# Optimization experiments

Hardware: AMD Instinct MI355X
Metric: run time of the kernel (lower is better)

Reference implementation:

```python
import jax, jax.numpy as jnp
import numpy as np

N_HEAD = 16
N_EMBD = 2048
HEAD_DIM = N_EMBD // N_HEAD
ROPE_BASE = 10000.0


def _rope_cos_sin(seq_len, dim, dtype):
    inv_freq = 1.0 / (ROPE_BASE ** (jnp.arange(0, dim, 2, dtype=jnp.float32) / dim))
    pos = jnp.arange(seq_len, dtype=jnp.float32)
    freqs = jnp.outer(pos, inv_freq)                 # [T, dim/2]
    emb = jnp.concatenate([freqs, freqs], axis=-1)   # [T, dim]
    return jnp.cos(emb).astype(dtype), jnp.sin(emb).astype(dtype)


def _rotate_half(x):
    x1, x2 = jnp.split(x, 2, axis=-1)
    return jnp.concatenate([-x2, x1], axis=-1)


def _apply_rotary(x, cos, sin):
    # x: [B, H, T, D]; cos/sin: [T, D] broadcast over B,H
    return x * cos[None, None] + _rotate_half(x) * sin[None, None]


def setup_inputs() -> dict:
    key = jax.random.key(0)
    ks = jax.random.split(key, 5)
    B, T, C = 4, 2048, N_EMBD
    s_in = 1.0 / np.sqrt(C)
    return {
        "x": jax.random.normal(ks[0], (B, T, C), dtype=jnp.float32),
        "W_attn": jax.random.normal(ks[1], (C, 3 * C), dtype=jnp.float32) * s_in,
        "b_attn": jax.random.normal(ks[2], (3 * C,), dtype=jnp.float32) * 0.02,
        "W_proj": jax.random.normal(ks[3], (C, C), dtype=jnp.float32) * s_in,
        "b_proj": jax.random.normal(ks[4], (C,), dtype=jnp.float32) * 0.02,
    }


def reference(x, W_attn, b_attn, W_proj, b_proj):
    B, T, C = x.shape
    H, D = N_HEAD, HEAD_DIM
    qkv = x @ W_attn + b_attn                        # [B, T, 3C]
    q, k, v = jnp.split(qkv, 3, axis=2)
    q = q.reshape(B, T, H, D).transpose(0, 2, 1, 3)  # [B, H, T, D]
    k = k.reshape(B, T, H, D).transpose(0, 2, 1, 3)
    v = v.reshape(B, T, H, D).transpose(0, 2, 1, 3)

    cos, sin = _rope_cos_sin(T, D, x.dtype)
    q = _apply_rotary(q, cos, sin)
    k = _apply_rotary(k, cos, sin)

    scale = 1.0 / jnp.sqrt(jnp.asarray(D, dtype=x.dtype))
    scores = jnp.einsum('bhqd,bhkd->bhqk', q, k) * scale
    causal = jnp.tril(jnp.ones((T, T), dtype=bool))
    scores = jnp.where(causal[None, None], scores, jnp.finfo(x.dtype).min)
    attn = jax.nn.softmax(scores, axis=-1)
    y = jnp.einsum('bhqk,bhkd->bhqd', attn, v)       # [B, H, T, D]
    y = y.transpose(0, 2, 1, 3).reshape(B, T, C)
    out = y @ W_proj + b_proj                        # dropout p=0 (eval)
    return out, k, v
```

## Files before the change

### kernel.cpp

```cpp
#include <hip/hip_runtime.h>


typedef __attribute__((ext_vector_type(4))) float f32x4;
typedef __attribute__((ext_vector_type(8))) __bf16 bf16x8;
typedef __attribute__((ext_vector_type(4))) unsigned short us4;

__device__ __forceinline__ unsigned short f2bf(float f) {
  unsigned u = __float_as_uint(f);
  u += 0x7FFFu + ((u >> 16) & 1u);
  return (unsigned short)(u >> 16);
}

__device__ __forceinline__ void gl_lds16(const void* g, void* l) {
  __builtin_amdgcn_global_load_lds(
      (const __attribute__((address_space(1))) void*)g,
      (__attribute__((address_space(3))) void*)l, 16, 0, 0);
}

__device__ __forceinline__ f32x4 mfma_bf16(bf16x8 a, bf16x8 b, f32x4 c) {
  return __builtin_amdgcn_mfma_f32_16x16x32_bf16(a, b, c, 0, 0, 0);
}


__global__ __launch_bounds__(256) void rope_table_kernel(float* __restrict__ cos_t,
                                                         float* __restrict__ sin_t) {
  int idx = blockIdx.x * 256 + threadIdx.x;
  int t = idx >> 6, i = idx & 63;
  float freq = __expf(-(float)i * 0.14391156831212787f);
  float ang = (float)t * freq;
  float s, c;
  sincosf(ang, &s, &c);
  cos_t[idx] = c;
  sin_t[idx] = s;
}

__global__ __launch_bounds__(256) void conv_bf16_kernel(const float* __restrict__ in,
                                                        unsigned short* __restrict__ out,
                                                        int n4) {
  int idx = blockIdx.x * 256 + threadIdx.x;
  int stride = gridDim.x * 256;
  for (; idx < n4; idx += stride) {
    float4 v = ((const float4*)in)[idx];
    us4 o;
    o[0] = f2bf(v.x); o[1] = f2bf(v.y); o[2] = f2bf(v.z); o[3] = f2bf(v.w);
    ((us4*)out)[idx] = o;
  }
}

__global__ __launch_bounds__(256) void transpose_conv_kernel(const float* __restrict__ in,
                                                             unsigned short* __restrict__ out,
                                                             int R, int C, int permute) {
  __shared__ unsigned short tile[64][68];
  const int t = threadIdx.x;
  const int c0 = blockIdx.x * 64, r0 = blockIdx.y * 64;
  const int cq = t & 15, rr = t >> 4;
#pragma unroll
  for (int i = 0; i < 4; ++i) {
    int r = rr + i * 16;
    float4 v = *(const float4*)&in[(size_t)(r0 + r) * C + c0 + cq * 4];
    tile[r][cq * 4 + 0] = f2bf(v.x);
    tile[r][cq * 4 + 1] = f2bf(v.y);
    tile[r][cq * 4 + 2] = f2bf(v.z);
    tile[r][cq * 4 + 3] = f2bf(v.w);
  }
  __syncthreads();
#pragma unroll
  for (int ii = 0; ii < 4; ++ii) {
    int c = rr + ii * 16;
    int n = c0 + c;
    int np = n;
    if (permute && n < 4096) {
      int d = n & 127, blk = d >> 5;
      int dd = (blk == 1) ? d + 32 : (blk == 2) ? d - 32 : d;
      np = (n & ~127) | dd;
    }
    us4 o;
#pragma unroll
    for (int jj = 0; jj < 4; ++jj) o[jj] = tile[cq * 4 + jj][c];
    *(us4*)&out[(size_t)np * R + r0 + cq * 4] = o;
  }
}

__global__ __launch_bounds__(256) void vtrans_kernel(const float* __restrict__ in,
                                                     unsigned short* __restrict__ out) {
  __shared__ unsigned short tile[64][68];
  const int t = threadIdx.x;
  const int t0 = blockIdx.x * 64;
  const int d0 = blockIdx.y * 64;
  const size_t zi = (size_t)blockIdx.z * 2048 * 128;
  const size_t zo = (size_t)blockIdx.z * 128 * 2048;
  const int cq = t & 15, rr = t >> 4;
#pragma unroll
  for (int i = 0; i < 4; ++i) {
    int r = rr + i * 16;
    float4 v = *(const float4*)&in[zi + (size_t)(t0 + r) * 128 + d0 + cq * 4];
    tile[r][cq * 4 + 0] = f2bf(v.x);
    tile[r][cq * 4 + 1] = f2bf(v.y);
    tile[r][cq * 4 + 2] = f2bf(v.z);
    tile[r][cq * 4 + 3] = f2bf(v.w);
  }
  __syncthreads();
#pragma unroll
  for (int ii = 0; ii < 4; ++ii) {
    int c = rr + ii * 16;
    us4 o;
#pragma unroll
    for (int jj = 0; jj < 4; ++jj) o[jj] = tile[cq * 4 + jj][c];
    *(us4*)&out[zo + (size_t)(d0 + c) * 2048 + t0 + cq * 4] = o;
  }
}


#define BARR __builtin_amdgcn_s_barrier()
#define LGKM                                                                   \
  do {                                                                         \
    asm volatile("s_waitcnt lgkmcnt(0)" ::: "memory");                         \
    __builtin_amdgcn_sched_barrier(0);                                         \
  } while (0)
#define WAITV(N) asm volatile("s_waitcnt vmcnt(" #N ")" ::: "memory")

#define STAGE_A_HALF(BUF, T, H)                                                \
  do {                                                                         \
    const int k0_ = (T) * 64;                                                  \
    _Pragma("unroll") for (int i_ = 0; i_ < 2; ++i_) {                         \
      int c_ = i_ * 512 + tid;                                                 \
      int rp_ = c_ >> 3, s_ = c_ & 7;                                          \
      int row_ = (rp_ & 63) + (H) * 64 + (rp_ >> 6) * 128;                     \
      gl_lds16(Ag + (size_t)row_ * 2048 + k0_ + ((s_ ^ (row_ & 7)) << 3),      \
               &As[BUF][row_ * 64 + s_ * 8]);                                  \
    }                                                                          \
  } while (0)

#define STAGE_B_HALF(BUF, T, H)                                                \
  do {                                                                         \
    const int k0_ = (T) * 64;                                                  \
    _Pragma("unroll") for (int i_ = 0; i_ < 2; ++i_) {                         \
      int c_ = i_ * 512 + tid;                                                 \
      int rp_ = c_ >> 3, s_ = c_ & 7;                                          \
      int row_ = (rp_ & 31) + (H) * 32 + (rp_ >> 5) * 64;                      \
      gl_lds16(Bg + (size_t)row_ * 2048 + k0_ + ((s_ ^ (row_ & 7)) << 3),      \
               &Bs[BUF][row_ * 64 + s_ * 8]);                                  \
    }                                                                          \
  } while (0)

#define LDA(mh)                                                                \
  _Pragma("unroll") for (int m2_ = 0; m2_ < 4; ++m2_)                          \
  _Pragma("unroll") for (int kk_ = 0; kk_ < 2; ++kk_) {                        \
    int R_ = wm * 128 + (mh) * 64 + m2_ * 16 + ln;                             \
    av[m2_][kk_] = *(const bf16x8*)&Ab[R_ * 64 +                               \
        (((kk_ * 64 + g * 16) ^ ((R_ & 7) << 4)) >> 1)];                       \
  }

#define LDB2                                                                   \
  _Pragma("unroll") for (int nh_ = 0; nh_ < 2; ++nh_)                          \
  _Pragma("unroll") for (int n2_ = 0; n2_ < 2; ++n2_)                          \
  _Pragma("unroll") for (int kk_ = 0; kk_ < 2; ++kk_) {                        \
    int R_ = wn * 64 + nh_ * 32 + n2_ * 16 + ln;                               \
    bv[nh_ * 2 + n2_][kk_] = *(const bf16x8*)&Bb[R_ * 64 +                     \
        (((kk_ * 64 + g * 16) ^ ((R_ & 7) << 4)) >> 1)];                       \
  }

#define MF16(mh, nh)                                                           \
  do {                                                                         \
    __builtin_amdgcn_s_setprio(1);                                             \
    _Pragma("unroll") for (int m2_ = 0; m2_ < 4; ++m2_)                        \
    _Pragma("unroll") for (int n2_ = 0; n2_ < 2; ++n2_)                        \
    _Pragma("unroll") for (int kk_ = 0; kk_ < 2; ++kk_)                        \
      acc[(mh) * 4 + m2_][(nh) * 2 + n2_] = mfma_bf16(                         \
          av[m2_][kk_], bv[(nh) * 2 + n2_][kk_],                               \
          acc[(mh) * 4 + m2_][(nh) * 2 + n2_]);                                \
    __builtin_amdgcn_s_setprio(0);                                             \
  } while (0)

#define GEMM_ENGINE_4PH(NT)                                                    \
  STAGE_A_HALF(0, 0, 0); STAGE_B_HALF(0, 0, 0);                                \
  STAGE_B_HALF(0, 0, 1); STAGE_A_HALF(0, 0, 1);                                \
  for (int t = 0; t < (NT); ++t) {                                             \
    const int p_ = t & 1, q_ = p_ ^ 1;                                         \
    const unsigned short* Ab = &As[p_][0];                                     \
    const unsigned short* Bb = &Bs[p_][0];                                     \
    const bool pf_ = (t + 1 < (NT));                                           \
    WAITV(2);                                                                  \
    BARR;                                                                      \
                                \
    LDB2; LDA(0);                                                              \
    if (pf_) STAGE_A_HALF(q_, t + 1, 0);                                       \
    LGKM;                                                                      \
    MF16(0, 0);                                                                \
                                             \
    if (pf_) STAGE_B_HALF(q_, t + 1, 0);                                       \
    MF16(0, 1);                                                                \
    if (pf_) { WAITV(4); } else { WAITV(0); }                                  \
    BARR;                                                                      \
                                        \
    LDA(1);                                                                    \
    if (pf_) STAGE_B_HALF(q_, t + 1, 1);                                       \
    LGKM;                                                                      \
    MF16(1, 0);                                                                \
                                             \
    if (pf_) STAGE_A_HALF(q_, t + 1, 1);                                       \
    MF16(1, 1);                                                                \
  }

__global__ __launch_bounds__(512, 2) void gemm_qkv_kernel(
    const unsigned short* __restrict__ xbf, const unsigned short* __restrict__ wt,
    const float* __restrict__ bias, const float* __restrict__ cost,
    const float* __restrict__ sint, float* __restrict__ out_k,
    float* __restrict__ out_v, unsigned short* __restrict__ qbf,
    unsigned short* __restrict__ kbf) {
  __shared__ __attribute__((aligned(16))) unsigned short As[2][256 * 64];
  __shared__ __attribute__((aligned(16))) unsigned short Bs[2][256 * 64];
  const int tid = threadIdx.x;
  const int wid = tid >> 6, l = tid & 63, g = l >> 4, ln = l & 15;
  const int wm = wid >> 2, wn = wid & 3;
  const int xcd = blockIdx.x & 7, local = blockIdx.x >> 3;
  const int mtile = xcd * 4 + (local & 3);
  const int ntile = local >> 2;
  const unsigned short* Ag = xbf + (size_t)(mtile * 256) * 2048;
  const unsigned short* Bg = wt + (size_t)(ntile * 256) * 2048;

  f32x4 acc[8][4];
#pragma unroll
  for (int i = 0; i < 8; ++i)
#pragma unroll
    for (int j = 0; j < 4; ++j) acc[i][j] = (f32x4){0.f, 0.f, 0.f, 0.f};
  bf16x8 av[4][2], bv[4][2];

  GEMM_ENGINE_4PH(32);

  const int colb = ntile * 256 + wn * 64;
  const int p = colb >> 11;
  const int h = (colb >> 7) & 15;
  const int Mb = mtile * 256 + wm * 128;

  if (p == 2) {
    float bvv[4];
#pragma unroll
    for (int nf = 0; nf < 4; ++nf) bvv[nf] = bias[colb + nf * 16 + ln];
    const int dbase = (wn & 1) * 64;
#pragma unroll
    for (int mf = 0; mf < 8; ++mf)
#pragma unroll
      for (int r = 0; r < 4; ++r) {
        int m = Mb + mf * 16 + g * 4 + r;
        int b = m >> 11, t = m & 2047;
        size_t base = ((size_t)(b * 16 + h) * 2048 + t) * 128;
#pragma unroll
        for (int nf = 0; nf < 4; ++nf)
          out_v[base + dbase + nf * 16 + ln] = acc[mf][nf][r] + bvv[nf];
      }
  } else {
    const float sc = 0.08838834764831845f;
    const int half32 = (wn & 1) * 32;
    float blo[2], bhi[2];
#pragma unroll
    for (int nf = 0; nf < 2; ++nf) {
      int d_lo = half32 + nf * 16 + ln;
      blo[nf] = bias[p * 2048 + h * 128 + d_lo];
      bhi[nf] = bias[p * 2048 + h * 128 + d_lo + 64];
    }
#pragma unroll
    for (int mf = 0; mf < 8; ++mf)
#pragma unroll
      for (int r = 0; r < 4; ++r) {
        int m = Mb + mf * 16 + g * 4 + r;
        int b = m >> 11, t = m & 2047;
        size_t base = ((size_t)(b * 16 + h) * 2048 + t) * 128;
#pragma unroll
        for (int nf = 0; nf < 2; ++nf) {
          int d_lo = half32 + nf * 16 + ln;
          float cv = cost[t * 64 + d_lo], sv = sint[t * 64 + d_lo];
          float a = acc[mf][nf][r] + blo[nf];
          float bq = acc[mf][nf + 2][r] + bhi[nf];
          float lo = a * cv - bq * sv;
          float hi = bq * cv + a * sv;
          if (p == 0) {
            qbf[base + d_lo] = f2bf(lo * sc);
            qbf[base + d_lo + 64] = f2bf(hi * sc);
          } else {
            out_k[base + d_lo] = lo;
            out_k[base + d_lo + 64] = hi;
            kbf[base + d_lo] = f2bf(lo);
            kbf[base + d_lo + 64] = f2bf(hi);
          }
        }
      }
  }
}

__global__ __launch_bounds__(512, 2) void gemm_proj_kernel(
    const unsigned short* __restrict__ ybf, const unsigned short* __restrict__ wpt,
    const float* __restrict__ bias, float* __restrict__ out) {
  __shared__ __attribute__((aligned(16))) unsigned short As[2][256 * 64];
  __shared__ __attribute__((aligned(16))) unsigned short Bs[2][256 * 64];
  const int tid = threadIdx.x;
  const int wid = tid >> 6, l = tid & 63, g = l >> 4, ln = l & 15;
  const int wm = wid >> 2, wn = wid & 3;
  const int xcd = blockIdx.x & 7, local = blockIdx.x >> 3;
  const int mtile = xcd * 4 + (local & 3);
  const int ntile = local >> 2;
  const unsigned short* Ag = ybf + (size_t)(mtile * 256) * 2048;
  const unsigned short* Bg = wpt + (size_t)(ntile * 256) * 2048;

  f32x4 acc[8][4];
#pragma unroll
  for (int i = 0; i < 8; ++i)
#pragma unroll
    for (int j = 0; j < 4; ++j) acc[i][j] = (f32x4){0.f, 0.f, 0.f, 0.f};
  bf16x8 av[4][2], bv[4][2];

  GEMM_ENGINE_4PH(32);

  const int n0 = ntile * 256 + wn * 64;
  const int Mb = mtile * 256 + wm * 128;
  float bvv[4];
#pragma unroll
  for (int nf = 0; nf < 4; ++nf) bvv[nf] = bias[n0 + nf * 16 + ln];
#pragma unroll
  for (int mf = 0; mf < 8; ++mf)
#pragma unroll
    for (int r = 0; r < 4; ++r) {
      int m = Mb + mf * 16 + g * 4 + r;
      size_t rb = (size_t)m * 2048 + n0;
#pragma unroll
      for (int nf = 0; nf < 4; ++nf)
        out[rb + nf * 16 + ln] = acc[mf][nf][r] + bvv[nf];
    }
}

__global__ __launch_bounds__(256, 2) void attn_kernel(
    const unsigned short* __restrict__ qbf, const unsigned short* __restrict__ kbf,
    const unsigned short* __restrict__ vtbf, unsigned short* __restrict__ ybf) {
  __shared__ __attribute__((aligned(16))) unsigned short Ks[2][64 * 128];
  __shared__ __attribute__((aligned(16))) unsigned short Vs[2][128 * 64];
  __shared__ __attribute__((aligned(16))) __bf16 Ps[4][32 * 64];
  const int tid = threadIdx.x;
  const int w = tid >> 6, l = tid & 63, g = l >> 4, ln = l & 15;
  const int bid = blockIdx.x;
  const int z = (bid & 7) * 8 + ((bid >> 3) & 7);
  const int qp = 15 - (bid >> 6);
  const size_t zo = (size_t)z * (2048 * 128);
  const size_t zv = (size_t)z * (128 * 2048);
  const int Q0w = qp * 128 + w * 32;
  const int jn = 2 * qp + 2;
  const int jlw = 2 * qp + (w >> 1);
  __bf16* Pw = Ps[w];

  bf16x8 qv[2][4];
#pragma unroll
  for (int mf = 0; mf < 2; ++mf)
#pragma unroll
    for (int kk = 0; kk < 4; ++kk)
      qv[mf][kk] = *(const bf16x8*)
          &qbf[zo + (size_t)(Q0w + mf * 16 + ln) * 128 + kk * 32 + g * 8];

  f32x4 o[2][8];
#pragma unroll
  for (int mf = 0; mf < 2; ++mf)
#pragma unroll
    for (int nf = 0; nf < 8; ++nf) o[mf][nf] = (f32x4){0.f, 0.f, 0.f, 0.f};
  float mrun[2][4], lrun[2][4];
#pragma unroll
  for (int mf = 0; mf < 2; ++mf)
#pragma unroll
    for (int r = 0; r < 4; ++r) { mrun[mf][r] = -3e38f; lrun[mf][r] = 0.f; }

#define STAGE_KV(J, B)                                                         \
  do {                                                                         \
    const int kv0_ = (J) << 6;                                                 \
    _Pragma("unroll") for (int i_ = 0; i_ < 4; ++i_) {                         \
      int c_ = i_ * 256 + tid;                                                 \
      int r_ = c_ >> 4, s_ = c_ & 15;                                          \
      gl_lds16(kbf + zo + (size_t)(kv0_ + r_) * 128 +                          \
                   (((s_ * 16) ^ ((r_ & 7) << 4)) >> 1),                       \
               &Ks[B][c_ * 8]);                                                \
    }                                                                          \
    _Pragma("unroll") for (int i_ = 0; i_ < 4; ++i_) {                         \
      int c_ = i_ * 256 + tid;                                                 \
      int d_ = c_ >> 3, s_ = c_ & 7;                                           \
      gl_lds16(vtbf + zv + (size_t)d_ * 2048 + kv0_ +                          \
                   (((s_ * 16) ^ ((d_ & 7) << 4)) >> 1),                       \
               &Vs[B][c_ * 8]);                                                \
    }                                                                          \
  } while (0)

  STAGE_KV(0, 0);
  STAGE_KV(1, 1);

  for (int j = 0; j < jn; ++j) {
    if (j + 1 < jn)
      asm volatile("s_waitcnt vmcnt(8)" ::: "memory");
    else
      asm volatile("s_waitcnt vmcnt(0)" ::: "memory");
    __builtin_amdgcn_s_barrier();
    const int bfr = j & 1;
    const unsigned short* Kb = Ks[bfr];
    const unsigned short* Vb = Vs[bfr];

    if (j <= jlw) {
      const int kv0 = j << 6;
      f32x4 s[2][4];
#pragma unroll
      for (int mf = 0; mf < 2; ++mf)
#pragma unroll
        for (int nf = 0; nf < 4; ++nf) s[mf][nf] = (f32x4){0.f, 0.f, 0.f, 0.f};
#pragma unroll
      for (int kk = 0; kk < 4; ++kk) {
        bf16x8 kf[4];
#pragma unroll
        for (int nf = 0; nf < 4; ++nf) {
          int rr = nf * 16 + ln;
          kf[nf] = *(const bf16x8*)
              &Kb[rr * 128 + (((kk * 64 + g * 16) ^ ((rr & 7) << 4)) >> 1)];
        }
#pragma unroll
        for (int mf = 0; mf < 2; ++mf)
#pragma unroll
          for (int nf = 0; nf < 4; ++nf)
            s[mf][nf] = mfma_bf16(qv[mf][kk], kf[nf], s[mf][nf]);
      }

      if (j == jlw) {
#pragma unroll
        for (int mf = 0; mf < 2; ++mf)
#pragma unroll
          for (int nf = 0; nf < 4; ++nf)
#pragma unroll
            for (int r = 0; r < 4; ++r)
              if (kv0 + nf * 16 + ln > Q0w + mf * 16 + g * 4 + r)
                s[mf][nf][r] = -3e38f;
      }

      float mx[2][4];
#pragma unroll
      for (int mf = 0; mf < 2; ++mf)
#pragma unroll
        for (int r = 0; r < 4; ++r) {
          float m0 = fmaxf(fmaxf(s[mf][0][r], s[mf][1][r]),
                           fmaxf(s[mf][2][r], s[mf][3][r]));
          m0 = fmaxf(m0, __shfl_xor(m0, 1));
          m0 = fmaxf(m0, __shfl_xor(m0, 2));
          m0 = fmaxf(m0, __shfl_xor(m0, 4));
          m0 = fmaxf(m0, __shfl_xor(m0, 8));
          mx[mf][r] = m0;
        }

      float dm = 0.f;
#pragma unroll
      for (int mf = 0; mf < 2; ++mf)
#pragma unroll
        for (int r = 0; r < 4; ++r) dm = fmaxf(dm, mx[mf][r] - mrun[mf][r]);
      if (__any(dm > 8.0f)) {
#pragma unroll
        for (int mf = 0; mf < 2; ++mf)
#pragma unroll
          for (int r = 0; r < 4; ++r) {
            float mn = fmaxf(mrun[mf][r], mx[mf][r]);
            float al = __expf(mrun[mf][r] - mn);
            mrun[mf][r] = mn;
            lrun[mf][r] *= al;
#pragma unroll
            for (int nf = 0; nf < 8; ++nf) o[mf][nf][r] *= al;
          }
      }

#pragma unroll
      for (int mf = 0; mf < 2; ++mf)
#pragma unroll
        for (int r = 0; r < 4; ++r) {
          const float m0 = mrun[mf][r];
          const int row_l = mf * 16 + g * 4 + r;
          float rs = 0.f;
#pragma unroll
          for (int nf = 0; nf < 4; ++nf) {
            float pv = __expf(s[mf][nf][r] - m0);
            rs += pv;
            int byte = ((nf * 16 + ln) << 1) ^ ((row_l & 7) << 4);
            Pw[row_l * 64 + (byte >> 1)] = (__bf16)pv;
          }
          rs += __shfl_xor(rs, 1);
          rs += __shfl_xor(rs, 2);
          rs += __shfl_xor(rs, 4);
          rs += __shfl_xor(rs, 8);
          lrun[mf][r] += rs;
        }

      asm volatile("s_waitcnt lgkmcnt(0)" ::: "memory");
      __builtin_amdgcn_sched_barrier(0);

#pragma unroll
      for (int kk2 = 0; kk2 < 2; ++kk2) {
        bf16x8 pa[2];
#pragma unroll
        for (int mf = 0; mf < 2; ++mf) {
          int pr = mf * 16 + ln;
          int byte = (kk2 * 64 + g * 16) ^ ((pr & 7) << 4);
          pa[mf] = *(const bf16x8*)&Pw[pr * 64 + (byte >> 1)];
        }
#pragma unroll
        for (int nf2 = 0; nf2 < 8; ++nf2) {
          int dr = nf2 * 16 + ln;
          bf16x8 vf = *(const bf16x8*)
              &Vb[dr * 64 + (((kk2 * 64 + g * 16) ^ ((dr & 7) << 4)) >> 1)];
#pragma unroll
          for (int mf = 0; mf < 2; ++mf)
            o[mf][nf2] = mfma_bf16(pa[mf], vf, o[mf][nf2]);
        }
      }
    }

    __builtin_amdgcn_s_barrier();
    __builtin_amdgcn_sched_barrier(0);
    if (j + 2 < jn) STAGE_KV(j + 2, bfr);
  }
#undef STAGE_KV

  const int b = z >> 4, h = z & 15;
#pragma unroll
  for (int mf = 0; mf < 2; ++mf)
#pragma unroll
    for (int r = 0; r < 4; ++r) {
      float inv = 1.f / lrun[mf][r];
      int t = Q0w + mf * 16 + g * 4 + r;
      size_t rb = ((size_t)b * 2048 + t) * 2048 + h * 128;
#pragma unroll
      for (int nf2 = 0; nf2 < 8; ++nf2)
        ybf[rb + nf2 * 16 + ln] = f2bf(o[mf][nf2][r] * inv);
    }
}

extern "C" void kernel_launch(void* const* d_in, const int* in_sizes, int n_in,
                              void* d_out, int out_size, void* d_ws, size_t ws_size,
                              hipStream_t stream) {
  (void)in_sizes; (void)n_in; (void)out_size; (void)ws_size;
  const float* x      = (const float*)d_in[0];
  const float* W_attn = (const float*)d_in[1];
  const float* b_attn = (const float*)d_in[2];
  const float* W_proj = (const float*)d_in[3];
  const float* b_proj = (const float*)d_in[4];

  float* out   = (float*)d_out;
  float* out_k = out + 16777216;
  float* out_v = out + 33554432;

  char* ws = (char*)d_ws;
  unsigned short* q_bf  = (unsigned short*)(ws + 0);
  unsigned short* k_bf  = (unsigned short*)(ws + 33554432);
  unsigned short* vt_bf = (unsigned short*)(ws + 67108864);
  unsigned short* x_bf  = (unsigned short*)(ws + 100663296);
  unsigned short* y2d   = x_bf;
  unsigned short* wt    = (unsigned short*)(ws + 134217728);
  unsigned short* wpt   = (unsigned short*)(ws + 159383552);
  float* cos_t = (float*)(ws + 167772160);
  float* sin_t = (float*)(ws + 168296448);

  rope_table_kernel<<<512, 256, 0, stream>>>(cos_t, sin_t);
  conv_bf16_kernel<<<2048, 256, 0, stream>>>(x, x_bf, 16777216 / 4);
  transpose_conv_kernel<<<dim3(6144 / 64, 2048 / 64), 256, 0, stream>>>(W_attn, wt, 2048, 6144, 1);
  transpose_conv_kernel<<<dim3(2048 / 64, 2048 / 64), 256, 0, stream>>>(W_proj, wpt, 2048, 2048, 0);
  gemm_qkv_kernel<<<768, 512, 0, stream>>>(x_bf, wt, b_attn, cos_t, sin_t,
                                           out_k, out_v, q_bf, k_bf);
  vtrans_kernel<<<dim3(32, 2, 64), 256, 0, stream>>>(out_v, vt_bf);
  attn_kernel<<<1024, 256, 0, stream>>>(q_bf, k_bf, vt_bf, y2d);
  gemm_proj_kernel<<<256, 512, 0, stream>>>(y2d, wpt, b_proj, out);
}
```

Before: 456.0 us.

## Restructure GEMM main loop to single barrier with upfront fragment loads

Measured after the change: 472.9 us. 1.04x slower.

```diff
diff --git a/kernel.cpp b/kernel.cpp
--- a/kernel.cpp
+++ b/kernel.cpp
@@ -111,13 +111,7 @@
 }
 
 
-#define BARR __builtin_amdgcn_s_barrier()
-#define LGKM                                                                   \
-  do {                                                                         \
-    asm volatile("s_waitcnt lgkmcnt(0)" ::: "memory");                         \
-    __builtin_amdgcn_sched_barrier(0);                                         \
-  } while (0)
-#define WAITV(N) asm volatile("s_waitcnt vmcnt(" #N ")" ::: "memory")
+#define SCHEDB __builtin_amdgcn_sched_barrier(0)
 
 #define STAGE_A_HALF(BUF, T, H)                                                \
   do {                                                                         \
@@ -143,11 +137,11 @@
     }                                                                          \
   } while (0)
 
-#define LDA(mh)                                                                \
+#define LDA(mh, AV)                                                            \
   _Pragma("unroll") for (int m2_ = 0; m2_ < 4; ++m2_)                          \
   _Pragma("unroll") for (int kk_ = 0; kk_ < 2; ++kk_) {                        \
     int R_ = wm * 128 + (mh) * 64 + m2_ * 16 + ln;                             \
-    av[m2_][kk_] = *(const bf16x8*)&Ab[R_ * 64 +                               \
+    AV[m2_][kk_] = *(const bf16x8*)&Ab[R_ * 64 +                               \
         (((kk_ * 64 + g * 16) ^ ((R_ & 7) << 4)) >> 1)];                       \
   }
 
@@ -160,19 +154,19 @@
         (((kk_ * 64 + g * 16) ^ ((R_ & 7) << 4)) >> 1)];                       \
   }
 
-#define MF16(mh, nh)                                                           \
+#define MF16(mh, nh, AV)                                                       \
   do {                                                                         \
     __builtin_amdgcn_s_setprio(1);                                             \
     _Pragma("unroll") for (int m2_ = 0; m2_ < 4; ++m2_)                        \
     _Pragma("unroll") for (int n2_ = 0; n2_ < 2; ++n2_)                        \
     _Pragma("unroll") for (int kk_ = 0; kk_ < 2; ++kk_)                        \
       acc[(mh) * 4 + m2_][(nh) * 2 + n2_] = mfma_bf16(                         \
-          av[m2_][kk_], bv[(nh) * 2 + n2_][kk_],                               \
+          AV[m2_][kk_], bv[(nh) * 2 + n2_][kk_],                               \
           acc[(mh) * 4 + m2_][(nh) * 2 + n2_]);                                \
     __builtin_amdgcn_s_setprio(0);                                             \
   } while (0)
 
-#define GEMM_ENGINE_4PH(NT)                                                    \
+#define GEMM_ENGINE_1B(NT)                                                     \
   STAGE_A_HALF(0, 0, 0); STAGE_B_HALF(0, 0, 0);                                \
   STAGE_B_HALF(0, 0, 1); STAGE_A_HALF(0, 0, 1);                                \
   for (int t = 0; t < (NT); ++t) {                                             \
@@ -180,26 +174,22 @@
     const unsigned short* Ab = &As[p_][0];                                     \
     const unsigned short* Bb = &Bs[p_][0];                                     \
     const bool pf_ = (t + 1 < (NT));                                           \
-    WAITV(2);                                                                  \
-    BARR;                                                                      \
-                                \
-    LDB2; LDA(0);                                                              \
-    if (pf_) STAGE_A_HALF(q_, t + 1, 0);                                       \
-    LGKM;                                                                      \
-    MF16(0, 0);                                                                \
-                                             \
-    if (pf_) STAGE_B_HALF(q_, t + 1, 0);                                       \
-    MF16(0, 1);                                                                \
-    if (pf_) { WAITV(4); } else { WAITV(0); }                                  \
-    BARR;                                                                      \
-                                        \
-    LDA(1);                                                                    \
-    if (pf_) STAGE_B_HALF(q_, t + 1, 1);                                       \
-    LGKM;                                                                      \
-    MF16(1, 0);                                                                \
-                                             \
-    if (pf_) STAGE_A_HALF(q_, t + 1, 1);                                       \
-    MF16(1, 1);                                                                \
+    __syncthreads();    \
+    LDB2; LDA(0, av0);                                \
+    SCHEDB;                           \
+    LDA(1, av1);                                       \
+    if (pf_) {                                                                 \
+      STAGE_A_HALF(q_, t + 1, 0); STAGE_B_HALF(q_, t + 1, 0);                  \
+      STAGE_B_HALF(q_, t + 1, 1); STAGE_A_HALF(q_, t + 1, 1);                  \
+    }                                                                          \
+    asm volatile("s_waitcnt lgkmcnt(8)" ::: "memory");                         \
+    SCHEDB;                                                                    \
+    MF16(0, 0, av0);                                                           \
+    MF16(0, 1, av0);                                                           \
+    asm volatile("s_waitcnt lgkmcnt(0)" ::: "memory");                         \
+    SCHEDB;                                                                    \
+    MF16(1, 0, av1);                                                           \
+    MF16(1, 1, av1);                                                           \
   }
 
 __global__ __launch_bounds__(512, 2) void gemm_qkv_kernel(
@@ -224,9 +214,9 @@
   for (int i = 0; i < 8; ++i)
 #pragma unroll
     for (int j = 0; j < 4; ++j) acc[i][j] = (f32x4){0.f, 0.f, 0.f, 0.f};
-  bf16x8 av[4][2], bv[4][2];
-
-  GEMM_ENGINE_4PH(32);
+  bf16x8 av0[4][2], av1[4][2], bv[4][2];
+
+  GEMM_ENGINE_1B(32);
 
   const int colb = ntile * 256 + wn * 64;
   const int p = colb >> 11;
@@ -307,9 +297,9 @@
   for (int i = 0; i < 8; ++i)
 #pragma unroll
     for (int j = 0; j < 4; ++j) acc[i][j] = (f32x4){0.f, 0.f, 0.f, 0.f};
-  bf16x8 av[4][2], bv[4][2];
-
-  GEMM_ENGINE_4PH(32);
+  bf16x8 av0[4][2], av1[4][2], bv[4][2];
+
+  GEMM_ENGINE_1B(32);
 
   const int n0 = ntile * 256 + wn * 64;
   const int Mb = mtile * 256 + wm * 128;
```

## Fuse V transpose into QKV GEMM epilogue and use exp2 softmax

Applied to the files above, without the earlier changes.

New measurement: 469.1 us. +2.9%, slower.

```diff
diff --git a/kernel.cpp b/kernel.cpp
--- a/kernel.cpp
+++ b/kernel.cpp
@@ -78,35 +78,6 @@
 #pragma unroll
     for (int jj = 0; jj < 4; ++jj) o[jj] = tile[cq * 4 + jj][c];
     *(us4*)&out[(size_t)np * R + r0 + cq * 4] = o;
-  }
-}
-
-__global__ __launch_bounds__(256) void vtrans_kernel(const float* __restrict__ in,
-                                                     unsigned short* __restrict__ out) {
-  __shared__ unsigned short tile[64][68];
-  const int t = threadIdx.x;
-  const int t0 = blockIdx.x * 64;
-  const int d0 = blockIdx.y * 64;
-  const size_t zi = (size_t)blockIdx.z * 2048 * 128;
-  const size_t zo = (size_t)blockIdx.z * 128 * 2048;
-  const int cq = t & 15, rr = t >> 4;
-#pragma unroll
-  for (int i = 0; i < 4; ++i) {
-    int r = rr + i * 16;
-    float4 v = *(const float4*)&in[zi + (size_t)(t0 + r) * 128 + d0 + cq * 4];
-    tile[r][cq * 4 + 0] = f2bf(v.x);
-    tile[r][cq * 4 + 1] = f2bf(v.y);
-    tile[r][cq * 4 + 2] = f2bf(v.z);
-    tile[r][cq * 4 + 3] = f2bf(v.w);
-  }
-  __syncthreads();
-#pragma unroll
-  for (int ii = 0; ii < 4; ++ii) {
-    int c = rr + ii * 16;
-    us4 o;
-#pragma unroll
-    for (int jj = 0; jj < 4; ++jj) o[jj] = tile[cq * 4 + jj][c];
-    *(us4*)&out[zo + (size_t)(d0 + c) * 2048 + t0 + cq * 4] = o;
   }
 }
 
@@ -207,7 +178,7 @@
     const float* __restrict__ bias, const float* __restrict__ cost,
     const float* __restrict__ sint, float* __restrict__ out_k,
     float* __restrict__ out_v, unsigned short* __restrict__ qbf,
-    unsigned short* __restrict__ kbf) {
+    unsigned short* __restrict__ kbf, unsigned short* __restrict__ vtb) {
   __shared__ __attribute__((aligned(16))) unsigned short As[2][256 * 64];
   __shared__ __attribute__((aligned(16))) unsigned short Bs[2][256 * 64];
   const int tid = threadIdx.x;
@@ -239,18 +210,27 @@
     for (int nf = 0; nf < 4; ++nf) bvv[nf] = bias[colb + nf * 16 + ln];
     const int dbase = (wn & 1) * 64;
 #pragma unroll
-    for (int mf = 0; mf < 8; ++mf)
-#pragma unroll
-      for (int r = 0; r < 4; ++r) {
-        int m = Mb + mf * 16 + g * 4 + r;
-        int b = m >> 11, t = m & 2047;
-        size_t base = ((size_t)(b * 16 + h) * 2048 + t) * 128;
-#pragma unroll
-        for (int nf = 0; nf < 4; ++nf)
-          out_v[base + dbase + nf * 16 + ln] = acc[mf][nf][r] + bvv[nf];
+    for (int mf = 0; mf < 8; ++mf) {
+      int t0 = Mb + mf * 16 + g * 4;
+      int b = t0 >> 11, t = t0 & 2047;
+      const int z = b * 16 + h;
+      size_t base = ((size_t)z * 2048 + t) * 128;
+      size_t vtz = (size_t)z * (128 * 2048);
+#pragma unroll
+      for (int nf = 0; nf < 4; ++nf) {
+        int d = dbase + nf * 16 + ln;
+        us4 pack;
+#pragma unroll
+        for (int r = 0; r < 4; ++r) {
+          float val = acc[mf][nf][r] + bvv[nf];
+          out_v[base + (size_t)r * 128 + d] = val;
+          pack[r] = f2bf(val);
+        }
+        *(us4*)&vtb[vtz + (size_t)d * 2048 + t] = pack;
       }
+    }
   } else {
-    const float sc = 0.08838834764831845f;
+    const float sc2 = 0.12751743681128098f;
     const int half32 = (wn & 1) * 32;
     float blo[2], bhi[2];
 #pragma unroll
@@ -275,8 +255,8 @@
           float lo = a * cv - bq * sv;
           float hi = bq * cv + a * sv;
           if (p == 0) {
-            qbf[base + d_lo] = f2bf(lo * sc);
-            qbf[base + d_lo + 64] = f2bf(hi * sc);
+            qbf[base + d_lo] = f2bf(lo * sc2);
+            qbf[base + d_lo + 64] = f2bf(hi * sc2);
           } else {
             out_k[base + d_lo] = lo;
             out_k[base + d_lo + 64] = hi;
@@ -450,13 +430,13 @@
       for (int mf = 0; mf < 2; ++mf)
 #pragma unroll
         for (int r = 0; r < 4; ++r) dm = fmaxf(dm, mx[mf][r] - mrun[mf][r]);
-      if (__any(dm > 8.0f)) {
+      if (__any(dm > 11.5416f)) {
 #pragma unroll
         for (int mf = 0; mf < 2; ++mf)
 #pragma unroll
           for (int r = 0; r < 4; ++r) {
             float mn = fmaxf(mrun[mf][r], mx[mf][r]);
-            float al = __expf(mrun[mf][r] - mn);
+            float al = exp2f(mrun[mf][r] - mn);
             mrun[mf][r] = mn;
             lrun[mf][r] *= al;
 #pragma unroll
@@ -473,7 +453,7 @@
           float rs = 0.f;
 #pragma unroll
           for (int nf = 0; nf < 4; ++nf) {
-            float pv = __expf(s[mf][nf][r] - m0);
+            float pv = exp2f(s[mf][nf][r] - m0);
             rs += pv;
             int byte = ((nf * 16 + ln) << 1) ^ ((row_l & 7) << 4);
             Pw[row_l * 64 + (byte >> 1)] = (__bf16)pv;
@@ -559,8 +539,7 @@
   transpose_conv_kernel<<<dim3(6144 / 64, 2048 / 64), 256, 0, stream>>>(W_attn, wt, 2048, 6144, 1);
   transpose_conv_kernel<<<dim3(2048 / 64, 2048 / 64), 256, 0, stream>>>(W_proj, wpt, 2048, 2048, 0);
   gemm_qkv_kernel<<<768, 512, 0, stream>>>(x_bf, wt, b_attn, cos_t, sin_t,
-                                           out_k, out_v, q_bf, k_bf);
-  vtrans_kernel<<<dim3(32, 2, 64), 256, 0, stream>>>(out_v, vt_bf);
+                                           out_k, out_v, q_bf, k_bf, vt_bf);
   attn_kernel<<<1024, 256, 0, stream>>>(q_bf, k_bf, vt_bf, y2d);
   gemm_proj_kernel<<<256, 512, 0, stream>>>(y2d, wpt, b_proj, out);
 }
```
